# Performance work log

Hardware: AMD Instinct MI355X
Metric: run time of the kernel (lower is better)

Reference implementation:

```python
import jax, jax.numpy as jnp
import numpy as np

N = 100000   # nodes
E = 1600000  # edges (before self loops)
H = 2        # attention heads
C = 32       # per-head channels
EPS_BN = 1e-5
NEG_SLOPE = 0.2


def setup_inputs():
    key = jax.random.key(0)
    ks = jax.random.split(key, 32)
    s = 0.1
    inp = {
        "h": jax.random.normal(ks[0], (N, 2), jnp.float32),
        "edge_index": jax.random.randint(ks[1], (2, E), 0, N, dtype=jnp.int32),
        "bn_gamma": jnp.ones((2,), jnp.float32),
        "bn_beta": jnp.zeros((2,), jnp.float32),
        # GATConv 1: in=2 -> H*C=64
        "W1": jax.random.normal(ks[2], (H * C, 2), jnp.float32) * s,
        "as1": jax.random.normal(ks[3], (H, C), jnp.float32) * s,
        "ad1": jax.random.normal(ks[4], (H, C), jnp.float32) * s,
        "b1": jnp.zeros((H * C,), jnp.float32),
        # GATConv 2: in=64 -> 64
        "W2": jax.random.normal(ks[5], (H * C, 64), jnp.float32) * s,
        "as2": jax.random.normal(ks[6], (H, C), jnp.float32) * s,
        "ad2": jax.random.normal(ks[7], (H, C), jnp.float32) * s,
        "b2": jnp.zeros((H * C,), jnp.float32),
    }
    dims = [(64, 64), (64, 64), (64, 64), (64, 64), (11, 64)]
    for i, (o, ii) in enumerate(dims, start=1):
        inp[f"fw{i}"] = jax.random.normal(ks[8 + 2 * i], (o, ii), jnp.float32) * s
        inp[f"fb{i}"] = jnp.zeros((o,), jnp.float32)
    return inp


def _gat_layer(x, src, dst, W, a_src, a_dst, b):
    # x: [N, Fin] -> xp: [N, H, C]
    xp = (x @ W.T).reshape(N, H, C)
    e_src = jnp.einsum("nhc,hc->nh", xp, a_src)  # [N,H]
    e_dst = jnp.einsum("nhc,hc->nh", xp, a_dst)
    e = jax.nn.leaky_relu(e_src[src] + e_dst[dst], NEG_SLOPE)  # [Etot,H]
    # segment softmax over incoming edges of each dst node
    m = jax.ops.segment_max(e, dst, num_segments=N)            # [N,H]
    ex = jnp.exp(e - m[dst])
    denom = jax.ops.segment_sum(ex, dst, num_segments=N)
    alpha = ex / (denom[dst] + 1e-16)                          # [Etot,H]
    out = jax.ops.segment_sum(xp[src] * alpha[:, :, None], dst, num_segments=N)
    return out.reshape(N, H * C) + b


def reference(h, edge_index, bn_gamma, bn_beta,
              W1, as1, ad1, b1, W2, as2, ad2, b2,
              fw1, fb1, fw2, fb2, fw3, fb3, fw4, fb4, fw5, fb5):
    # BatchNorm1d (training mode: batch statistics, biased variance)
    mu = h.mean(0)
    var = ((h - mu) ** 2).mean(0)
    x = (h - mu) * jax.lax.rsqrt(var + EPS_BN) * bn_gamma + bn_beta

    # add self loops (PyG GATConv default)
    ar = jnp.arange(N, dtype=edge_index.dtype)
    src = jnp.concatenate([edge_index[0], ar])
    dst = jnp.concatenate([edge_index[1], ar])

    x = jax.nn.relu(_gat_layer(x, src, dst, W1, as1, ad1, b1))
    x = jax.nn.relu(_gat_layer(x, src, dst, W2, as2, ad2, b2))

    x = jax.nn.relu(x @ fw1.T + fb1)
    x = jax.nn.relu(x @ fw2.T + fb2)
    x = jax.nn.relu(x @ fw3.T + fb3)
    x = jax.nn.relu(x @ fw4.T + fb4)
    return x @ fw5.T + fb5
```

## Files before the change

kernel.cpp:

```cpp
#include <hip/hip_runtime.h>
#include <hip/hip_fp16.h>
#include <math.h>

#define NN 100000
#define EE 1600000
#define ET (EE + NN)
#define NEG 0.2f
#define SMASK 0x1FFFF

#define NBUCK 196
#define NBLK 416
#define BITEMS 4096
#define BCAP 10240

typedef float4 f4;
typedef _Float16 h8 __attribute__((ext_vector_type(8)));
typedef float f32x4 __attribute__((ext_vector_type(4)));

__global__ void k_init(float* stats, int* gcnt) {
    int i = threadIdx.x;
    if (i < 4) stats[i] = 0.f;
    if (i < NBUCK) gcnt[i] = 0;
}

__global__ void k_bnstats(const float* __restrict__ h, float* stats) {
    __shared__ float red[16];
    int gid = blockIdx.x * blockDim.x + threadIdx.x;
    int stride = gridDim.x * blockDim.x;
    float s0 = 0.f, s1 = 0.f, q0 = 0.f, q1 = 0.f;
    for (int i = gid; i < NN; i += stride) {
        float2 v = reinterpret_cast<const float2*>(h)[i];
        s0 += v.x; q0 += v.x * v.x;
        s1 += v.y; q1 += v.y * v.y;
    }
#pragma unroll
    for (int off = 32; off >= 1; off >>= 1) {
        s0 += __shfl_xor(s0, off);
        s1 += __shfl_xor(s1, off);
        q0 += __shfl_xor(q0, off);
        q1 += __shfl_xor(q1, off);
    }
    int wv = threadIdx.x >> 6;
    if ((threadIdx.x & 63) == 0) {
        red[wv * 4 + 0] = s0; red[wv * 4 + 1] = s1;
        red[wv * 4 + 2] = q0; red[wv * 4 + 3] = q1;
    }
    __syncthreads();
    if (threadIdx.x == 0) {
        float t0 = 0.f, t1 = 0.f, t2 = 0.f, t3 = 0.f;
#pragma unroll
        for (int i = 0; i < 4; ++i) {
            t0 += red[i * 4 + 0]; t1 += red[i * 4 + 1];
            t2 += red[i * 4 + 2]; t3 += red[i * 4 + 3];
        }
        atomicAdd(&stats[0], t0); atomicAdd(&stats[1], t1);
        atomicAdd(&stats[2], t2); atomicAdd(&stats[3], t3);
    }
}

__global__ void k_coef(const float* __restrict__ W1, const float* __restrict__ as1,
                       const float* __restrict__ ad1, float* __restrict__ coef) {
    int t = threadIdx.x;
    if (t >= 8) return;
    int sd = t >> 2, hh = (t >> 1) & 1, i = t & 1;
    const float* a = sd ? ad1 : as1;
    float s = 0.f;
    for (int c = 0; c < 32; ++c) s += W1[(hh * 32 + c) * 2 + i] * a[hh * 32 + c];
    coef[t] = s;
}

__global__ void k_wprep(const float* __restrict__ W2g,
                        const float* __restrict__ w1, const float* __restrict__ w2,
                        const float* __restrict__ w3, const float* __restrict__ w4,
                        const float* __restrict__ w5,
                        _Float16* __restrict__ BH, _Float16* __restrict__ BL,
                        _Float16* __restrict__ BH5, _Float16* __restrict__ BL5) {
    int idx = blockIdx.x * blockDim.x + threadIdx.x;
    if (idx < 5 * 4096) {
        int L = idx >> 12;
        int r = idx & 4095;
        int ks = r >> 11, nt = (r >> 9) & 3, lane = (r >> 3) & 63, j = r & 7;
        const float* W = (L == 0) ? w1 : (L == 1) ? w2 : (L == 2) ? w3 : (L == 3) ? w4 : W2g;
        int n = nt * 16 + (lane & 15);
        int k = ks * 32 + 8 * (lane >> 4) + j;
        float v = W[n * 64 + k];
        _Float16 hi = (_Float16)v;
        BH[idx] = hi;
        BL[idx] = (_Float16)(v - (float)hi);
    }
    if (idx < 1024) {
        int ks = idx >> 9, lane = (idx >> 3) & 63, j = idx & 7;
        int n = lane & 15;
        int k = ks * 32 + 8 * (lane >> 4) + j;
        float v = (n < 11) ? w5[n * 64 + k] : 0.f;
        _Float16 hi = (_Float16)v;
        BH5[idx] = hi;
        BL5[idx] = (_Float16)(v - (float)hi);
    }
}

__global__ void __launch_bounds__(256) k_fpart(const int* __restrict__ ei, int* gcnt,
                                               unsigned* __restrict__ pairs) {
    __shared__ int hist[NBUCK];
    __shared__ int cur[NBUCK];
    int tid = threadIdx.x, blk = blockIdx.x;
    if (tid < NBUCK) hist[tid] = 0;
    int ss[16], dd[16];
    int base = blk * BITEMS;
    __syncthreads();
#pragma unroll
    for (int it = 0; it < 16; ++it) {
        int i = base + it * 256 + tid;
        int s = 0, d = -1;
        if (i < ET) {
            if (i < EE) { s = ei[i]; d = ei[EE + i]; }
            else { s = d = i - EE; }
            atomicAdd(&hist[d >> 9], 1);
        }
        ss[it] = s; dd[it] = d;
    }
    __syncthreads();
    if (tid < NBUCK) cur[tid] = tid * BCAP + atomicAdd(&gcnt[tid], hist[tid]);
    __syncthreads();
#pragma unroll
    for (int it = 0; it < 16; ++it) {
        int d = dd[it];
        if (d >= 0) {
            int pos = atomicAdd(&cur[d >> 9], 1);
            pairs[pos] = (unsigned)ss[it] | ((unsigned)(d & 511) << 17);
        }
    }
}

__global__ void k_scan196(const int* __restrict__ gcnt, int* __restrict__ rboff) {
    __shared__ int sm[256];
    int tid = threadIdx.x;
    int v = (tid < NBUCK) ? gcnt[tid] : 0;
    sm[tid] = v;
    __syncthreads();
    for (int off = 1; off < 256; off <<= 1) {
        int t = (tid >= off) ? sm[tid - off] : 0;
        __syncthreads();
        sm[tid] += t;
        __syncthreads();
    }
    if (tid < NBUCK) rboff[tid] = sm[tid] - v;
    if (tid == 0) rboff[NBUCK] = ET;
}

__global__ void __launch_bounds__(512) k_bucket(const unsigned* __restrict__ pairs,
                                                 const int* __restrict__ gcnt,
                                                 const int* __restrict__ rboff,
                                                 int* __restrict__ rowptr,
                                                 unsigned* __restrict__ srcl) {
    __shared__ int sh[512];
    __shared__ int se[512];
    int b = blockIdx.x, tid = threadIdx.x;
    int cnt = gcnt[b];
    int ibase = b * BCAP;
    int obase = rboff[b];
    sh[tid] = 0;
    __syncthreads();
    for (int k = tid; k < cnt; k += 512) atomicAdd(&sh[pairs[ibase + k] >> 17], 1);
    __syncthreads();
    int deg = sh[tid];
    se[tid] = deg;
    __syncthreads();
    for (int off = 1; off < 512; off <<= 1) {
        int t = (tid >= off) ? se[tid - off] : 0;
        __syncthreads();
        se[tid] += t;
        __syncthreads();
    }
    int excl = se[tid] - deg;
    int node = (b << 9) + tid;
    if (node < NN) rowptr[node] = obase + excl;
    sh[tid] = obase + excl;
    __syncthreads();
    for (int k = tid; k < cnt; k += 512) {
        unsigned p = pairs[ibase + k];
        int pos = atomicAdd(&sh[p >> 17], 1);
        srcl[pos] = p;
    }
    if (b == 0 && tid == 0) rowptr[NN] = ET;
}

__global__ void k_prep1(const float* __restrict__ h, const float* __restrict__ stats,
                        const float* __restrict__ gamma, const float* __restrict__ beta,
                        const float* __restrict__ coef,
                        f4* __restrict__ nd1, float2* __restrict__ ed1) {
    int n = blockIdx.x * blockDim.x + threadIdx.x;
    if (n >= NN) return;
    const float inv = 1.f / (float)NN;
    float mu0 = stats[0] * inv, mu1 = stats[1] * inv;
    float v0 = stats[2] * inv - mu0 * mu0;
    float v1 = stats[3] * inv - mu1 * mu1;
    float g0 = rsqrtf(v0 + 1e-5f) * gamma[0];
    float g1 = rsqrtf(v1 + 1e-5f) * gamma[1];
    float2 hv = reinterpret_cast<const float2*>(h)[n];
    float x0 = (hv.x - mu0) * g0 + beta[0];
    float x1 = (hv.y - mu1) * g1 + beta[1];
    nd1[n] = make_float4(x0 * coef[0] + x1 * coef[1], x0 * coef[2] + x1 * coef[3], x0, x1);
    ed1[n] = make_float2(x0 * coef[4] + x1 * coef[5], x0 * coef[6] + x1 * coef[7]);
}

__global__ void __launch_bounds__(256) k_gat1(
    const f4* __restrict__ nd1, const float2* __restrict__ ed1,
    const int* __restrict__ rowptr, const unsigned* __restrict__ srcl,
    f4* __restrict__ agg1a, float2* __restrict__ agg1s) {
    int gid = blockIdx.x * blockDim.x + threadIdx.x;
    int n = gid >> 3;
    int sub = gid & 7;
    if (n >= NN) return;
    int beg = rowptr[n], end = rowptr[n + 1];
    float2 ed = ed1[n];
    float A0 = 0.f, B0 = 0.f, S0 = 0.f, A1 = 0.f, B1 = 0.f, S1 = 0.f;
    for (int k = beg + sub; k < end; k += 8) {
        int s = (int)(srcl[k] & SMASK);
        f4 p = nd1[s];
        float e0 = p.x + ed.x;
        float e1 = p.y + ed.y;
        e0 = (e0 > 0.f) ? e0 : NEG * e0;
        e1 = (e1 > 0.f) ? e1 : NEG * e1;
        float w0 = __expf(e0);
        float w1 = __expf(e1);
        A0 += w0 * p.z; B0 += w0 * p.w; S0 += w0;
        A1 += w1 * p.z; B1 += w1 * p.w; S1 += w1;
    }
#pragma unroll
    for (int off = 1; off < 8; off <<= 1) {
        A0 += __shfl_xor(A0, off);
        B0 += __shfl_xor(B0, off);
        S0 += __shfl_xor(S0, off);
        A1 += __shfl_xor(A1, off);
        B1 += __shfl_xor(B1, off);
        S1 += __shfl_xor(S1, off);
    }
    if (sub == 0) {
        agg1a[n] = make_float4(A0, B0, A1, B1);
        agg1s[n] = make_float2(S0, S1);
    }
}

#define MAKE_A(ks)                                                                \
    f4 a0 = *reinterpret_cast<const f4*>(&xw[mrow * 68 + kg * 8 + (ks) * 32]);    \
    f4 a1 = *reinterpret_cast<const f4*>(&xw[mrow * 68 + kg * 8 + (ks) * 32 + 4]);\
    float av0 = a0.x, av1 = a0.y, av2 = a0.z, av3 = a0.w;                         \
    float av4 = a1.x, av5 = a1.y, av6 = a1.z, av7 = a1.w;                         \
    h8 ah, al;                                                                    \
    { _Float16 t;                                                                 \
      t = (_Float16)av0; ah[0] = t; al[0] = (_Float16)(av0 - (float)t);           \
      t = (_Float16)av1; ah[1] = t; al[1] = (_Float16)(av1 - (float)t);           \
      t = (_Float16)av2; ah[2] = t; al[2] = (_Float16)(av2 - (float)t);           \
      t = (_Float16)av3; ah[3] = t; al[3] = (_Float16)(av3 - (float)t);           \
      t = (_Float16)av4; ah[4] = t; al[4] = (_Float16)(av4 - (float)t);           \
      t = (_Float16)av5; ah[5] = t; al[5] = (_Float16)(av5 - (float)t);           \
      t = (_Float16)av6; ah[6] = t; al[6] = (_Float16)(av6 - (float)t);           \
      t = (_Float16)av7; ah[7] = t; al[7] = (_Float16)(av7 - (float)t); }

__global__ void __launch_bounds__(256) k_xform2m(
    const f4* __restrict__ agg1a, const float2* __restrict__ agg1s,
    const float* __restrict__ W1, const float* __restrict__ b1,
    const _Float16* __restrict__ BH2, const _Float16* __restrict__ BL2,
    const float* __restrict__ a_s, const float* __restrict__ a_d,
    __half* __restrict__ xph, float2* __restrict__ es2v, float2* __restrict__ ed2v) {
    __shared__ float xs[4 * 1088];
    int lane = threadIdx.x & 63;
    int w = threadIdx.x >> 6;
    float* xw = &xs[w * 1088];
    int nodeBase = blockIdx.x * 64 + w * 16;
    int mrow = lane & 15;
    int kg = lane >> 4;
    int n = nodeBase + mrow;

    f4 ag = make_float4(0.f, 0.f, 0.f, 0.f);
    float2 sg = make_float2(1.f, 1.f);
    if (n < NN) { ag = agg1a[n]; sg = agg1s[n]; }
    float r0 = 1.f / (sg.x + 1e-16f);
    float r1 = 1.f / (sg.y + 1e-16f);
#pragma unroll
    for (int j = 0; j < 16; ++j) {
        int f = kg * 16 + j;
        float A = (f < 32) ? ag.x : ag.z;
        float B = (f < 32) ? ag.y : ag.w;
        float r = (f < 32) ? r0 : r1;
        xw[mrow * 68 + f] = fmaxf((A * W1[2 * f] + B * W1[2 * f + 1]) * r + b1[f], 0.f);
    }
    __syncthreads();

    const h8* bh = reinterpret_cast<const h8*>(BH2);
    const h8* bl = reinterpret_cast<const h8*>(BL2);
    h8 BHr[2][4], BLr[2][4];
#pragma unroll
    for (int ks = 0; ks < 2; ++ks)
#pragma unroll
        for (int nt = 0; nt < 4; ++nt) {
            BHr[ks][nt] = bh[(ks * 4 + nt) * 64 + lane];
            BLr[ks][nt] = bl[(ks * 4 + nt) * 64 + lane];
        }
    f32x4 acc0 = {0.f, 0.f, 0.f, 0.f}, acc1 = acc0, acc2 = acc0, acc3 = acc0;
#pragma unroll
    for (int ks = 0; ks < 2; ++ks) {
        MAKE_A(ks)
        acc0 = __builtin_amdgcn_mfma_f32_16x16x32_f16(ah, BHr[ks][0], acc0, 0, 0, 0);
        acc1 = __builtin_amdgcn_mfma_f32_16x16x32_f16(ah, BHr[ks][1], acc1, 0, 0, 0);
        acc2 = __builtin_amdgcn_mfma_f32_16x16x32_f16(ah, BHr[ks][2], acc2, 0, 0, 0);
        acc3 = __builtin_amdgcn_mfma_f32_16x16x32_f16(ah, BHr[ks][3], acc3, 0, 0, 0);
        acc0 = __builtin_amdgcn_mfma_f32_16x16x32_f16(ah, BLr[ks][0], acc0, 0, 0, 0);
        acc1 = __builtin_amdgcn_mfma_f32_16x16x32_f16(ah, BLr[ks][1], acc1, 0, 0, 0);
        acc2 = __builtin_amdgcn_mfma_f32_16x16x32_f16(ah, BLr[ks][2], acc2, 0, 0, 0);
        acc3 = __builtin_amdgcn_mfma_f32_16x16x32_f16(ah, BLr[ks][3], acc3, 0, 0, 0);
        acc0 = __builtin_amdgcn_mfma_f32_16x16x32_f16(al, BHr[ks][0], acc0, 0, 0, 0);
        acc1 = __builtin_amdgcn_mfma_f32_16x16x32_f16(al, BHr[ks][1], acc1, 0, 0, 0);
        acc2 = __builtin_amdgcn_mfma_f32_16x16x32_f16(al, BHr[ks][2], acc2, 0, 0, 0);
        acc3 = __builtin_amdgcn_mfma_f32_16x16x32_f16(al, BHr[ks][3], acc3, 0, 0, 0);
    }
    __syncthreads();
#pragma unroll
    for (int r = 0; r < 4; ++r) {
        int row = 4 * kg + r;
        xw[row * 68 + mrow]      = acc0[r];
        xw[row * 68 + 16 + mrow] = acc1[r];
        xw[row * 68 + 32 + mrow] = acc2[r];
        xw[row * 68 + 48 + mrow] = acc3[r];
    }
    __syncthreads();

    float ps = 0.f, pd = 0.f;
#pragma unroll
    for (int j = 0; j < 16; ++j) {
        int f = kg * 16 + j;
        float v = xw[mrow * 68 + f];
        ps += v * a_s[f];
        pd += v * a_d[f];
    }
    ps += __shfl_xor(ps, 16);
    pd += __shfl_xor(pd, 16);
    float psB = __shfl_xor(ps, 32);
    float pdB = __shfl_xor(pd, 32);
    if (kg == 0 && n < NN) {
        es2v[n] = make_float2(ps, psB);
        ed2v[n] = make_float2(pd, pdB);
    }

#pragma unroll
    for (int i = 0; i < 8; ++i) {
        int idx = lane + 64 * i;
        int nl = idx >> 5;
        int c = idx & 31;
        int g = nodeBase + nl;
        if (g < NN) {
            __half2 hv = __floats2half2_rn(xw[nl * 68 + 2 * c], xw[nl * 68 + 2 * c + 1]);
            *reinterpret_cast<__half2*>(&xph[(size_t)g * 64 + 2 * c]) = hv;
        }
    }
}

__global__ void __launch_bounds__(256) k_gat2(
    const __half* __restrict__ xph, const float2* __restrict__ es2v,
    const float2* __restrict__ ed2v,
    const int* __restrict__ rowptr, const unsigned* __restrict__ srcl,
    const float* __restrict__ bias, float* __restrict__ y) {
    int wid = (blockIdx.x * blockDim.x + threadIdx.x) >> 6;
    int lane = threadIdx.x & 63;
    if (wid >= NN) return;
    int l5 = lane & 31;
    int hs = lane >> 5;
    bool headhi = l5 >= 16;
    int ch = 2 * l5;
    float2 edp = ed2v[wid];
    float edv = headhi ? edp.y : edp.x;
    int beg = rowptr[wid], end = rowptr[wid + 1];
    float sum = 0.f, a0 = 0.f, a1 = 0.f;
    int k = beg;

#define GPAIR(kk)                                                                 \
    {                                                                             \
        int s_ = (int)(srcl[(kk) + hs] & SMASK);                                  \
        float2 ep_ = es2v[s_];                                                    \
        unsigned xr_ = *reinterpret_cast<const unsigned*>(&xph[(size_t)s_ * 64 + ch]); \
        float e_ = (headhi ? ep_.y : ep_.x) + edv;                                \
        e_ = (e_ > 0.f) ? e_ : NEG * e_;                                          \
        float w_ = __expf(e_);                                                    \
        float2 xv_ = __half22float2(*reinterpret_cast<const __half2*>(&xr_));     \
        sum += w_; a0 += w_ * xv_.x; a1 += w_ * xv_.y;                            \
    }

    for (; k + 16 <= end; k += 16) {
        GPAIR(k) GPAIR(k + 2) GPAIR(k + 4) GPAIR(k + 6)
        GPAIR(k + 8) GPAIR(k + 10) GPAIR(k + 12) GPAIR(k + 14)
    }
    for (; k + 8 <= end; k += 8) {
        GPAIR(k) GPAIR(k + 2) GPAIR(k + 4) GPAIR(k + 6)
    }
    for (; k < end; k += 2) {
        int idx = k + hs;
        bool valid = idx < end;
        int s_ = (int)(srcl[valid ? idx : k] & SMASK);
        float2 ep_ = es2v[s_];
        unsigned xr_ = *reinterpret_cast<const unsigned*>(&xph[(size_t)s_ * 64 + ch]);
        float e_ = (headhi ? ep_.y : ep_.x) + edv;
        e_ = (e_ > 0.f) ? e_ : NEG * e_;
        float w_ = valid ? __expf(e_) : 0.f;
        float2 xv_ = __half22float2(*reinterpret_cast<const __half2*>(&xr_));
        sum += w_; a0 += w_ * xv_.x; a1 += w_ * xv_.y;
    }
#undef GPAIR

    sum += __shfl_xor(sum, 32);
    a0  += __shfl_xor(a0, 32);
    a1  += __shfl_xor(a1, 32);
    if (lane < 32) {
        float rs = 1.f / (sum + 1e-16f);
        float r0 = fmaxf(a0 * rs + bias[ch], 0.f);
        float r1 = fmaxf(a1 * rs + bias[ch + 1], 0.f);
        *reinterpret_cast<float2*>(&y[(size_t)wid * 64 + ch]) = make_float2(r0, r1);
    }
}

__global__ void __launch_bounds__(256) k_mlp(
    const float* __restrict__ hin,
    const _Float16* __restrict__ BH, const _Float16* __restrict__ BL,
    const _Float16* __restrict__ BH5, const _Float16* __restrict__ BL5,
    const float* __restrict__ b1, const float* __restrict__ b2,
    const float* __restrict__ b3, const float* __restrict__ b4,
    const float* __restrict__ b5,
    float* __restrict__ out) {
    __shared__ float xs[4 * 16 * 68];
    int lane = threadIdx.x & 63;
    int w = threadIdx.x >> 6;
    float* xw = &xs[w * 1088];
    int nodeBase = blockIdx.x * 64 + w * 16;
    int mrow = lane & 15;
    int kg = lane >> 4;

#pragma unroll
    for (int i = 0; i < 4; ++i) {
        int v = lane + 64 * i;
        int nl = v >> 4;
        int c4 = v & 15;
        f4 t = make_float4(0.f, 0.f, 0.f, 0.f);
        if (nodeBase + nl < NN)
            t = reinterpret_cast<const f4*>(hin)[(size_t)(nodeBase + nl) * 16 + c4];
        *reinterpret_cast<f4*>(&xw[nl * 68 + c4 * 4]) = t;
    }
    __syncthreads();

#define MLP_LAYER(L, Bp)                                                          \
    {                                                                             \
        const h8* bh = reinterpret_cast<const h8*>(BH + (L) * 4096);              \
        const h8* bl = reinterpret_cast<const h8*>(BL + (L) * 4096);              \
        h8 BHr[2][4], BLr[2][4];                                                  \
        _Pragma("unroll")                                                         \
        for (int ks = 0; ks < 2; ++ks)                                            \
            _Pragma("unroll")                                                     \
            for (int nt = 0; nt < 4; ++nt) {                                      \
                BHr[ks][nt] = bh[(ks * 4 + nt) * 64 + lane];                      \
                BLr[ks][nt] = bl[(ks * 4 + nt) * 64 + lane];                      \
            }                                                                     \
        float bj0 = Bp[mrow], bj1 = Bp[16 + mrow];                                \
        float bj2 = Bp[32 + mrow], bj3 = Bp[48 + mrow];                           \
        f32x4 acc0 = {0.f, 0.f, 0.f, 0.f}, acc1 = acc0, acc2 = acc0, acc3 = acc0; \
        _Pragma("unroll")                                                         \
        for (int ks = 0; ks < 2; ++ks) {                                          \
            MAKE_A(ks)                                                            \
            acc0 = __builtin_amdgcn_mfma_f32_16x16x32_f16(ah, BHr[ks][0], acc0, 0, 0, 0); \
            acc1 = __builtin_amdgcn_mfma_f32_16x16x32_f16(ah, BHr[ks][1], acc1, 0, 0, 0); \
            acc2 = __builtin_amdgcn_mfma_f32_16x16x32_f16(ah, BHr[ks][2], acc2, 0, 0, 0); \
            acc3 = __builtin_amdgcn_mfma_f32_16x16x32_f16(ah, BHr[ks][3], acc3, 0, 0, 0); \
            acc0 = __builtin_amdgcn_mfma_f32_16x16x32_f16(ah, BLr[ks][0], acc0, 0, 0, 0); \
            acc1 = __builtin_amdgcn_mfma_f32_16x16x32_f16(ah, BLr[ks][1], acc1, 0, 0, 0); \
            acc2 = __builtin_amdgcn_mfma_f32_16x16x32_f16(ah, BLr[ks][2], acc2, 0, 0, 0); \
            acc3 = __builtin_amdgcn_mfma_f32_16x16x32_f16(ah, BLr[ks][3], acc3, 0, 0, 0); \
            acc0 = __builtin_amdgcn_mfma_f32_16x16x32_f16(al, BHr[ks][0], acc0, 0, 0, 0); \
            acc1 = __builtin_amdgcn_mfma_f32_16x16x32_f16(al, BHr[ks][1], acc1, 0, 0, 0); \
            acc2 = __builtin_amdgcn_mfma_f32_16x16x32_f16(al, BHr[ks][2], acc2, 0, 0, 0); \
            acc3 = __builtin_amdgcn_mfma_f32_16x16x32_f16(al, BHr[ks][3], acc3, 0, 0, 0); \
        }                                                                         \
        __syncthreads();                                                          \
        _Pragma("unroll")                                                         \
        for (int r = 0; r < 4; ++r) {                                             \
            int row = 4 * kg + r;                                                 \
            xw[row * 68 + mrow]      = fmaxf(acc0[r] + bj0, 0.f);                 \
            xw[row * 68 + 16 + mrow] = fmaxf(acc1[r] + bj1, 0.f);                 \
            xw[row * 68 + 32 + mrow] = fmaxf(acc2[r] + bj2, 0.f);                 \
            xw[row * 68 + 48 + mrow] = fmaxf(acc3[r] + bj3, 0.f);                 \
        }                                                                         \
        __syncthreads();                                                          \
    }

    MLP_LAYER(0, b1)
    MLP_LAYER(1, b2)
    MLP_LAYER(2, b3)
    MLP_LAYER(3, b4)
#undef MLP_LAYER

    {
        const h8* bh = reinterpret_cast<const h8*>(BH5);
        const h8* bl = reinterpret_cast<const h8*>(BL5);
        f32x4 acc = {0.f, 0.f, 0.f, 0.f};
#pragma unroll
        for (int ks = 0; ks < 2; ++ks) {
            MAKE_A(ks)
            h8 b_h = bh[ks * 64 + lane];
            h8 b_l = bl[ks * 64 + lane];
            acc = __builtin_amdgcn_mfma_f32_16x16x32_f16(ah, b_h, acc, 0, 0, 0);
            acc = __builtin_amdgcn_mfma_f32_16x16x32_f16(ah, b_l, acc, 0, 0, 0);
            acc = __builtin_amdgcn_mfma_f32_16x16x32_f16(al, b_h, acc, 0, 0, 0);
        }
        if (mrow < 11) {
            float b5v = b5[mrow];
#pragma unroll
            for (int r = 0; r < 4; ++r) {
                int node = nodeBase + 4 * kg + r;
                if (node < NN) out[(size_t)node * 11 + mrow] = acc[r] + b5v;
            }
        }
    }
}

extern "C" void kernel_launch(void* const* d_in, const int* in_sizes, int n_in,
                              void* d_out, int out_size, void* d_ws, size_t ws_size,
                              hipStream_t stream) {
    const float* h   = (const float*)d_in[0];
    const int*   ei  = (const int*)d_in[1];
    const float* gam = (const float*)d_in[2];
    const float* bet = (const float*)d_in[3];
    const float* W1  = (const float*)d_in[4];
    const float* as1 = (const float*)d_in[5];
    const float* ad1 = (const float*)d_in[6];
    const float* b1  = (const float*)d_in[7];
    const float* W2  = (const float*)d_in[8];
    const float* as2 = (const float*)d_in[9];
    const float* ad2 = (const float*)d_in[10];
    const float* b2  = (const float*)d_in[11];
    const float* fw1 = (const float*)d_in[12];
    const float* fb1 = (const float*)d_in[13];
    const float* fw2 = (const float*)d_in[14];
    const float* fb2 = (const float*)d_in[15];
    const float* fw3 = (const float*)d_in[16];
    const float* fb3 = (const float*)d_in[17];
    const float* fw4 = (const float*)d_in[18];
    const float* fb4 = (const float*)d_in[19];
    const float* fw5 = (const float*)d_in[20];
    const float* fb5 = (const float*)d_in[21];
    float* out = (float*)d_out;

    char* ws = (char*)d_ws;
    size_t off = 0;
    auto alloc = [&](size_t bytes) -> char* {
        char* p = ws + off;
        off += (bytes + 255) & ~(size_t)255;
        return p;
    };
    float* stats  = (float*)alloc(4 * sizeof(float));
    float* coef   = (float*)alloc(8 * sizeof(float));
    int*   gcnt   = (int*)alloc(NBUCK * sizeof(int));
    int*   rboff  = (int*)alloc((NBUCK + 1) * sizeof(int));
    int*   rowptr = (int*)alloc((size_t)(NN + 1) * sizeof(int));
    unsigned* srcl = (unsigned*)alloc((size_t)ET * sizeof(unsigned));
    float2* es2v  = (float2*)alloc((size_t)NN * sizeof(float2));
    float2* ed2v  = (float2*)alloc((size_t)NN * sizeof(float2));
    _Float16* BH  = (_Float16*)alloc(5 * 4096 * sizeof(_Float16));
    _Float16* BL  = (_Float16*)alloc(5 * 4096 * sizeof(_Float16));
    _Float16* BH5 = (_Float16*)alloc(1024 * sizeof(_Float16));
    _Float16* BL5 = (_Float16*)alloc(1024 * sizeof(_Float16));
    float* bufA   = (float*)alloc((size_t)NN * 64 * sizeof(float));
    float* bufB   = (float*)alloc((size_t)NN * 64 * sizeof(float));
    unsigned* pairs = (unsigned*)bufA;
    __half* xph   = (__half*)bufA;
    f4*     agg1a = (f4*)bufB;
    float2* agg1s = (float2*)(bufB + 400000);
    f4*     nd1   = (f4*)(bufB + 600000);
    float2* ed1   = (float2*)(bufB + 1000000);
    (void)ws_size; (void)in_sizes; (void)n_in; (void)out_size;

    k_init<<<1, 256, 0, stream>>>(stats, gcnt);
    k_bnstats<<<64, 256, 0, stream>>>(h, stats);
    k_coef<<<1, 64, 0, stream>>>(W1, as1, ad1, coef);
    k_wprep<<<96, 256, 0, stream>>>(W2, fw1, fw2, fw3, fw4, fw5, BH, BL, BH5, BL5);

    k_fpart<<<NBLK, 256, 0, stream>>>(ei, gcnt, pairs);
    k_scan196<<<1, 256, 0, stream>>>(gcnt, rboff);
    k_bucket<<<NBUCK, 512, 0, stream>>>(pairs, gcnt, rboff, rowptr, srcl);

    k_prep1<<<(NN + 255) / 256, 256, 0, stream>>>(h, stats, gam, bet, coef, nd1, ed1);
    k_gat1<<<(NN * 8 + 255) / 256, 256, 0, stream>>>(nd1, ed1, rowptr, srcl, agg1a, agg1s);

    k_xform2m<<<(NN + 63) / 64, 256, 0, stream>>>(agg1a, agg1s, W1, b1,
                                                  BH + 4 * 4096, BL + 4 * 4096,
                                                  as2, ad2, xph, es2v, ed2v);

    k_gat2<<<(NN * 64) / 256, 256, 0, stream>>>(xph, es2v, ed2v, rowptr, srcl, b2, bufB);

    k_mlp<<<(NN + 63) / 64, 256, 0, stream>>>(bufB, BH, BL, BH5, BL5,
                                              fb1, fb2, fb3, fb4, fb5, out);
}
```

Measured before the change: 172.0 us.

## Fuse coef and scan kernels away and widen GAT2 gather to four edges

The attention coefficient precompute moves into the init kernel, and the bucket-offset scan is replaced by a per-block reduction inside the bucket kernel. This removes two tiny kernel launches and their dependency gaps. The layer-2 aggregation now has each wave process four edges at once, with 16 lanes each loading 4 half channels (8-byte loads), to raise gather parallelism. Leaky ReLU is expressed with fmaxf. In exchange, every bucket block redundantly reduces up to 196 counts, and the wider reduction adds one extra shuffle step.

```diff
diff --git a/kernel.cpp b/kernel.cpp
--- a/kernel.cpp
+++ b/kernel.cpp
@@ -17,10 +17,20 @@
 typedef _Float16 h8 __attribute__((ext_vector_type(8)));
 typedef float f32x4 __attribute__((ext_vector_type(4)));
 
-__global__ void k_init(float* stats, int* gcnt) {
+__global__ void k_init(float* stats, int* gcnt,
+                       const float* __restrict__ W1, const float* __restrict__ as1,
+                       const float* __restrict__ ad1, float* __restrict__ coef) {
     int i = threadIdx.x;
     if (i < 4) stats[i] = 0.f;
     if (i < NBUCK) gcnt[i] = 0;
+    if (i >= 248) {
+        int t = i - 248;
+        int sd = t >> 2, hh = (t >> 1) & 1, c0 = t & 1;
+        const float* a = sd ? ad1 : as1;
+        float s = 0.f;
+        for (int c = 0; c < 32; ++c) s += W1[(hh * 32 + c) * 2 + c0] * a[hh * 32 + c];
+        coef[t] = s;
+    }
 }
 
 __global__ void k_bnstats(const float* __restrict__ h, float* stats) {
@@ -56,17 +66,6 @@
         atomicAdd(&stats[0], t0); atomicAdd(&stats[1], t1);
         atomicAdd(&stats[2], t2); atomicAdd(&stats[3], t3);
     }
-}
-
-__global__ void k_coef(const float* __restrict__ W1, const float* __restrict__ as1,
-                       const float* __restrict__ ad1, float* __restrict__ coef) {
-    int t = threadIdx.x;
-    if (t >= 8) return;
-    int sd = t >> 2, hh = (t >> 1) & 1, i = t & 1;
-    const float* a = sd ? ad1 : as1;
-    float s = 0.f;
-    for (int c = 0; c < 32; ++c) s += W1[(hh * 32 + c) * 2 + i] * a[hh * 32 + c];
-    coef[t] = s;
 }
 
 __global__ void k_wprep(const float* __restrict__ W2g,
@@ -132,33 +131,23 @@
     }
 }
 
-__global__ void k_scan196(const int* __restrict__ gcnt, int* __restrict__ rboff) {
-    __shared__ int sm[256];
-    int tid = threadIdx.x;
-    int v = (tid < NBUCK) ? gcnt[tid] : 0;
-    sm[tid] = v;
-    __syncthreads();
-    for (int off = 1; off < 256; off <<= 1) {
-        int t = (tid >= off) ? sm[tid - off] : 0;
-        __syncthreads();
-        sm[tid] += t;
-        __syncthreads();
-    }
-    if (tid < NBUCK) rboff[tid] = sm[tid] - v;
-    if (tid == 0) rboff[NBUCK] = ET;
-}
-
 __global__ void __launch_bounds__(512) k_bucket(const unsigned* __restrict__ pairs,
                                                  const int* __restrict__ gcnt,
-                                                 const int* __restrict__ rboff,
                                                  int* __restrict__ rowptr,
                                                  unsigned* __restrict__ srcl) {
     __shared__ int sh[512];
     __shared__ int se[512];
     int b = blockIdx.x, tid = threadIdx.x;
+    sh[tid] = (tid < b) ? gcnt[tid] : 0;
+    __syncthreads();
+    for (int off = 256; off >= 1; off >>= 1) {
+        if (tid < off) sh[tid] += sh[tid + off];
+        __syncthreads();
+    }
+    int obase = sh[0];
+    __syncthreads();
     int cnt = gcnt[b];
     int ibase = b * BCAP;
-    int obase = rboff[b];
     sh[tid] = 0;
     __syncthreads();
     for (int k = tid; k < cnt; k += 512) atomicAdd(&sh[pairs[ibase + k] >> 17], 1);
@@ -220,8 +209,8 @@
         f4 p = nd1[s];
         float e0 = p.x + ed.x;
         float e1 = p.y + ed.y;
-        e0 = (e0 > 0.f) ? e0 : NEG * e0;
-        e1 = (e1 > 0.f) ? e1 : NEG * e1;
+        e0 = fmaxf(e0, NEG * e0);
+        e1 = fmaxf(e1, NEG * e1);
         float w0 = __expf(e0);
         float w1 = __expf(e1);
         A0 += w0 * p.z; B0 += w0 * p.w; S0 += w0;
@@ -364,57 +353,68 @@
     int wid = (blockIdx.x * blockDim.x + threadIdx.x) >> 6;
     int lane = threadIdx.x & 63;
     if (wid >= NN) return;
-    int l5 = lane & 31;
-    int hs = lane >> 5;
-    bool headhi = l5 >= 16;
-    int ch = 2 * l5;
+    int g = lane >> 4;
+    int t = lane & 15;
+    bool hh = t >= 8;
+    int ch = 4 * t;
     float2 edp = ed2v[wid];
-    float edv = headhi ? edp.y : edp.x;
+    float edv = hh ? edp.y : edp.x;
     int beg = rowptr[wid], end = rowptr[wid + 1];
-    float sum = 0.f, a0 = 0.f, a1 = 0.f;
+    float sum = 0.f, a0 = 0.f, a1 = 0.f, a2 = 0.f, a3 = 0.f;
     int k = beg;
 
-#define GPAIR(kk)                                                                 \
+#define GQ(kk)                                                                    \
     {                                                                             \
-        int s_ = (int)(srcl[(kk) + hs] & SMASK);                                  \
+        int s_ = (int)(srcl[(kk) + g] & SMASK);                                   \
         float2 ep_ = es2v[s_];                                                    \
-        unsigned xr_ = *reinterpret_cast<const unsigned*>(&xph[(size_t)s_ * 64 + ch]); \
-        float e_ = (headhi ? ep_.y : ep_.x) + edv;                                \
-        e_ = (e_ > 0.f) ? e_ : NEG * e_;                                          \
+        uint2 xr_ = *reinterpret_cast<const uint2*>(&xph[(size_t)s_ * 64 + ch]);  \
+        float e_ = (hh ? ep_.y : ep_.x) + edv;                                    \
+        e_ = fmaxf(e_, NEG * e_);                                                 \
         float w_ = __expf(e_);                                                    \
-        float2 xv_ = __half22float2(*reinterpret_cast<const __half2*>(&xr_));     \
-        sum += w_; a0 += w_ * xv_.x; a1 += w_ * xv_.y;                            \
+        float2 xa_ = __half22float2(*reinterpret_cast<const __half2*>(&xr_.x));   \
+        float2 xb_ = __half22float2(*reinterpret_cast<const __half2*>(&xr_.y));   \
+        sum += w_;                                                                \
+        a0 += w_ * xa_.x; a1 += w_ * xa_.y; a2 += w_ * xb_.x; a3 += w_ * xb_.y;   \
     }
 
     for (; k + 16 <= end; k += 16) {
-        GPAIR(k) GPAIR(k + 2) GPAIR(k + 4) GPAIR(k + 6)
-        GPAIR(k + 8) GPAIR(k + 10) GPAIR(k + 12) GPAIR(k + 14)
-    }
-    for (; k + 8 <= end; k += 8) {
-        GPAIR(k) GPAIR(k + 2) GPAIR(k + 4) GPAIR(k + 6)
-    }
-    for (; k < end; k += 2) {
-        int idx = k + hs;
+        GQ(k) GQ(k + 4) GQ(k + 8) GQ(k + 12)
+    }
+    for (; k + 4 <= end; k += 4) {
+        GQ(k)
+    }
+    if (k < end) {
+        int idx = k + g;
         bool valid = idx < end;
         int s_ = (int)(srcl[valid ? idx : k] & SMASK);
         float2 ep_ = es2v[s_];
-        unsigned xr_ = *reinterpret_cast<const unsigned*>(&xph[(size_t)s_ * 64 + ch]);
-        float e_ = (headhi ? ep_.y : ep_.x) + edv;
-        e_ = (e_ > 0.f) ? e_ : NEG * e_;
+        uint2 xr_ = *reinterpret_cast<const uint2*>(&xph[(size_t)s_ * 64 + ch]);
+        float e_ = (hh ? ep_.y : ep_.x) + edv;
+        e_ = fmaxf(e_, NEG * e_);
         float w_ = valid ? __expf(e_) : 0.f;
-        float2 xv_ = __half22float2(*reinterpret_cast<const __half2*>(&xr_));
-        sum += w_; a0 += w_ * xv_.x; a1 += w_ * xv_.y;
-    }
-#undef GPAIR
-
-    sum += __shfl_xor(sum, 32);
-    a0  += __shfl_xor(a0, 32);
-    a1  += __shfl_xor(a1, 32);
-    if (lane < 32) {
+        float2 xa_ = __half22float2(*reinterpret_cast<const __half2*>(&xr_.x));
+        float2 xb_ = __half22float2(*reinterpret_cast<const __half2*>(&xr_.y));
+        sum += w_;
+        a0 += w_ * xa_.x; a1 += w_ * xa_.y; a2 += w_ * xb_.x; a3 += w_ * xb_.y;
+    }
+#undef GQ
+
+#pragma unroll
+    for (int off = 16; off <= 32; off <<= 1) {
+        sum += __shfl_xor(sum, off);
+        a0  += __shfl_xor(a0, off);
+        a1  += __shfl_xor(a1, off);
+        a2  += __shfl_xor(a2, off);
+        a3  += __shfl_xor(a3, off);
+    }
+    if (lane < 16) {
         float rs = 1.f / (sum + 1e-16f);
-        float r0 = fmaxf(a0 * rs + bias[ch], 0.f);
-        float r1 = fmaxf(a1 * rs + bias[ch + 1], 0.f);
-        *reinterpret_cast<float2*>(&y[(size_t)wid * 64 + ch]) = make_float2(r0, r1);
+        f4 r;
+        r.x = fmaxf(a0 * rs + bias[ch], 0.f);
+        r.y = fmaxf(a1 * rs + bias[ch + 1], 0.f);
+        r.z = fmaxf(a2 * rs + bias[ch + 2], 0.f);
+        r.w = fmaxf(a3 * rs + bias[ch + 3], 0.f);
+        *reinterpret_cast<f4*>(&y[(size_t)wid * 64 + ch]) = r;
     }
 }
 
@@ -556,7 +556,6 @@
     float* stats  = (float*)alloc(4 * sizeof(float));
     float* coef   = (float*)alloc(8 * sizeof(float));
     int*   gcnt   = (int*)alloc(NBUCK * sizeof(int));
-    int*   rboff  = (int*)alloc((NBUCK + 1) * sizeof(int));
     int*   rowptr = (int*)alloc((size_t)(NN + 1) * sizeof(int));
     unsigned* srcl = (unsigned*)alloc((size_t)ET * sizeof(unsigned));
     float2* es2v  = (float2*)alloc((size_t)NN * sizeof(float2));
@@ -575,14 +574,12 @@
     float2* ed1   = (float2*)(bufB + 1000000);
     (void)ws_size; (void)in_sizes; (void)n_in; (void)out_size;
 
-    k_init<<<1, 256, 0, stream>>>(stats, gcnt);
+    k_init<<<1, 256, 0, stream>>>(stats, gcnt, W1, as1, ad1, coef);
     k_bnstats<<<64, 256, 0, stream>>>(h, stats);
-    k_coef<<<1, 64, 0, stream>>>(W1, as1, ad1, coef);
     k_wprep<<<96, 256, 0, stream>>>(W2, fw1, fw2, fw3, fw4, fw5, BH, BL, BH5, BL5);
 
     k_fpart<<<NBLK, 256, 0, stream>>>(ei, gcnt, pairs);
-    k_scan196<<<1, 256, 0, stream>>>(gcnt, rboff);
-    k_bucket<<<NBUCK, 512, 0, stream>>>(pairs, gcnt, rboff, rowptr, srcl);
+    k_bucket<<<NBUCK, 512, 0, stream>>>(pairs, gcnt, rowptr, srcl);
 
     k_prep1<<<(NN + 255) / 256, 256, 0, stream>>>(h, stats, gam, bet, coef, nd1, ed1);
     k_gat1<<<(NN * 8 + 255) / 256, 256, 0, stream>>>(nd1, ed1, rowptr, srcl, agg1a, agg1s);
```

New measurement: 159.6 us. 1.08x faster.
